# Kernel tuning notes

Hardware: AMD Instinct MI355X
Metric: run time of the kernel (lower is better)

Reference implementation:

```python
import jax, jax.numpy as jnp
import numpy as np

RES = (160, 160, 160)
SCENE_MIN = -1.0
SCENE_SIZE = 2.0
NEAR, FAR = 0.1, 10.0
NUM_SAMPLES = 128


def eval_sh_deg2(dirs):
    # dirs: [N, 3] -> SH basis [N, 9] (degree 2)
    d = dirs / (jnp.linalg.norm(dirs, axis=-1, keepdims=True) + 1e-8)
    x, y, z = d[..., 0], d[..., 1], d[..., 2]
    return jnp.stack([
        0.28209479177387814 * jnp.ones_like(x),
        -0.48860251190291987 * y,
        0.48860251190291987 * z,
        -0.48860251190291987 * x,
        1.0925484305920792 * x * y,
        -1.0925484305920792 * y * z,
        0.31539156525252005 * (2.0 * z * z - x * x - y * y),
        -1.0925484305920792 * x * z,
        0.5462742152960396 * (x * x - y * y),
    ], axis=-1)


def trilinear_interp(coords, density, sh_coeffs):
    # coords: [N, 3] world coords; grids indexed [z, y, x] as in the torch source
    res = jnp.asarray(RES, dtype=coords.dtype)
    vox = (coords - SCENE_MIN) / SCENE_SIZE * res
    vox = jnp.clip(vox, 0.0, res - 1.0)
    fl = jnp.floor(vox)
    frac = vox - fl
    fl = fl.astype(jnp.int32)
    x0, y0, z0 = fl[..., 0], fl[..., 1], fl[..., 2]
    x1 = jnp.minimum(x0 + 1, RES[0] - 1)
    y1 = jnp.minimum(y0 + 1, RES[1] - 1)
    z1 = jnp.minimum(z0 + 1, RES[2] - 1)
    dx, dy, dz = frac[..., 0], frac[..., 1], frac[..., 2]
    corners = [
        ((z0, y0, x0), (1 - dx) * (1 - dy) * (1 - dz)),
        ((z1, y0, x0), (1 - dx) * (1 - dy) * dz),
        ((z0, y1, x0), (1 - dx) * dy * (1 - dz)),
        ((z1, y1, x0), (1 - dx) * dy * dz),
        ((z0, y0, x1), dx * (1 - dy) * (1 - dz)),
        ((z1, y0, x1), dx * (1 - dy) * dz),
        ((z0, y1, x1), dx * dy * (1 - dz)),
        ((z1, y1, x1), dx * dy * dz),
    ]
    dens = 0.0
    sh = 0.0
    for (zi, yi, xi), w in corners:
        dens = dens + w * density[zi, yi, xi]
        sh = sh + w[:, None, None] * sh_coeffs[zi, yi, xi]
    return dens, sh


def plenoxel_forward(ray_origins, ray_directions, density, sh_coeffs):
    R = ray_origins.shape[0]
    t_vals = jnp.linspace(NEAR, FAR, NUM_SAMPLES, dtype=ray_origins.dtype)  # [S]
    # points: [R, S, 3]
    points = ray_origins[:, None, :] + t_vals[None, :, None] * ray_directions[:, None, :]
    pts = points.reshape(-1, 3)
    dens, sh = trilinear_interp(pts, density, sh_coeffs)  # [N], [N,3,9]
    dirs = jnp.broadcast_to(ray_directions[:, None, :], points.shape).reshape(-1, 3)
    basis = eval_sh_deg2(dirs)  # [N, 9]
    colors = jax.nn.sigmoid(jnp.sum(sh * basis[:, None, :], axis=-1))  # [N, 3]
    dens = dens.reshape(R, NUM_SAMPLES)
    colors = colors.reshape(R, NUM_SAMPLES, 3)
    # volume rendering
    dists = t_vals[1:] - t_vals[:-1]
    dists = jnp.concatenate([dists, jnp.full((1,), 1e10, dtype=t_vals.dtype)], axis=0)
    dists = dists[None, :] * jnp.linalg.norm(ray_directions, axis=-1, keepdims=True)  # [R,S]
    alpha = 1.0 - jnp.exp(-jax.nn.relu(dens) * dists)
    trans = jnp.cumprod(1.0 - alpha + 1e-10, axis=-1)
    trans = jnp.concatenate([jnp.ones_like(trans[..., :1]), trans[..., :-1]], axis=-1)
    weights = alpha * trans
    rgb = jnp.sum(weights[..., None] * colors, axis=-2)  # [R,3]
    depth = jnp.sum(weights * t_vals[None, :], axis=-1)  # [R]
    acc = jnp.sum(weights, axis=-1)  # [R]
    return rgb, depth, acc


def setup_inputs() -> dict:
    key = jax.random.key(0)
    k0, k1, k2, k3 = jax.random.split(key, 4)
    R = 4096
    ray_origins = jax.random.uniform(k0, (R, 3), dtype=jnp.float32, minval=-0.5, maxval=0.5)
    ray_directions = jax.random.normal(k1, (R, 3), dtype=jnp.float32)
    ray_directions = ray_directions / jnp.linalg.norm(ray_directions, axis=-1, keepdims=True)
    density = jax.random.uniform(k2, RES, dtype=jnp.float32, minval=-0.1, maxval=0.1)
    sh_coeffs = jax.random.uniform(k3, (*RES, 3, 9), dtype=jnp.float32, minval=-0.1, maxval=0.1)
    sh_coeffs = sh_coeffs.at[..., 0].set(0.5)
    return {"ray_origins": ray_origins, "ray_directions": ray_directions,
            "density": density, "sh_coeffs": sh_coeffs}


def reference(ray_origins, ray_directions, density, sh_coeffs):
    return plenoxel_forward(ray_origins, ray_directions, density, sh_coeffs)
```

## Files before the change

kernel.cpp:

```cpp
#include <hip/hip_runtime.h>
#include <math.h>

#define RES 160
#define NSAMP 128
#define NEAR_T 0.1f
#define FAR_T 10.0f

typedef float float4v __attribute__((ext_vector_type(4)));

__global__ __launch_bounds__(1024) void plenoxel_kernel(
    const float* __restrict__ ray_o,
    const float* __restrict__ ray_d,
    const float* __restrict__ density,
    const float* __restrict__ sh,
    float* __restrict__ out_rgb,
    float* __restrict__ out_depth,
    float* __restrict__ out_acc,
    int R)
{
    const int r   = blockIdx.x;
    const int tid = threadIdx.x;
    const int s   = tid >> 3;
    const int e   = tid & 7;
    if (r >= R) return;

    const float ox = ray_o[r * 3 + 0], oy = ray_o[r * 3 + 1], oz = ray_o[r * 3 + 2];
    const float dx = ray_d[r * 3 + 0], dy = ray_d[r * 3 + 1], dz = ray_d[r * 3 + 2];

    const float dn  = sqrtf(dx * dx + dy * dy + dz * dz);
    const float inv = 1.0f / (dn + 1e-8f);
    const float nx = dx * inv, ny = dy * inv, nz = dz * inv;
    const float b0 = 0.28209479177387814f;
    const float b1 = -0.48860251190291987f * ny;
    const float b2 =  0.48860251190291987f * nz;
    const float b3 = -0.48860251190291987f * nx;
    const float b4 =  1.0925484305920792f * nx * ny;
    const float b5 = -1.0925484305920792f * ny * nz;
    const float b6 =  0.31539156525252005f * (2.0f * nz * nz - nx * nx - ny * ny);
    const float b7 = -1.0925484305920792f * nx * nz;
    const float b8 =  0.5462742152960396f * (nx * nx - ny * ny);

    float4v bLo = {0.f, 0.f, 0.f, 0.f}, bHi = {0.f, 0.f, 0.f, 0.f};
    int chLo = 3, chHi = 3;
    switch (e) {
        case 0: bLo = (float4v){b0, b1, b2, b3}; chLo = 0; break;
        case 1: bLo = (float4v){b4, b5, b6, b7}; chLo = 0; break;
        case 2: bLo = (float4v){b8, 0.f, 0.f, 0.f}; bHi = (float4v){0.f, b0, b1, b2};
                chLo = 0; chHi = 1; break;
        case 3: bLo = (float4v){b3, b4, b5, b6}; chLo = 1; break;
        case 4: bLo = (float4v){b7, b8, 0.f, 0.f}; bHi = (float4v){0.f, 0.f, b0, b1};
                chLo = 1; chHi = 2; break;
        case 5: bLo = (float4v){b2, b3, b4, b5}; chLo = 2; break;
        case 6: bLo = (float4v){0.f, b6, b7, b8}; chLo = 2; break;
        default: break;
    }
    const int offE = (e >= 6) ? 23 : 4 * e;

    const float step = (FAR_T - NEAR_T) / (float)(NSAMP - 1);
    const float t = NEAR_T + step * (float)s;
    const float px = ox + t * dx, py = oy + t * dy, pz = oz + t * dz;
    float vx = (px + 1.0f) * 0.5f * (float)RES;
    float vy = (py + 1.0f) * 0.5f * (float)RES;
    float vz = (pz + 1.0f) * 0.5f * (float)RES;
    vx = fminf(fmaxf(vx, 0.0f), (float)(RES - 1));
    vy = fminf(fmaxf(vy, 0.0f), (float)(RES - 1));
    vz = fminf(fmaxf(vz, 0.0f), (float)(RES - 1));
    const float flx = floorf(vx), fly = floorf(vy), flz = floorf(vz);
    const int x0 = (int)flx, y0 = (int)fly, z0 = (int)flz;
    const int x1 = min(x0 + 1, RES - 1);
    const int y1 = min(y0 + 1, RES - 1);
    const int z1 = min(z0 + 1, RES - 1);
    const float fx = vx - flx, fy = vy - fly, fz = vz - flz;

    const float wx0 = 1.0f - fx, wx1 = fx;
    const float wy0 = 1.0f - fy, wy1 = fy;
    const float wz0 = 1.0f - fz, wz1 = fz;

    const int zy00 = (z0 * RES + y0) * RES;
    const int zy01 = (z0 * RES + y1) * RES;
    const int zy10 = (z1 * RES + y0) * RES;
    const int zy11 = (z1 * RES + y1) * RES;
    int   vidx[8];
    float w8[8];
    vidx[0] = zy00 + x0; w8[0] = wx0 * wy0 * wz0;
    vidx[1] = zy10 + x0; w8[1] = wx0 * wy0 * wz1;
    vidx[2] = zy01 + x0; w8[2] = wx0 * wy1 * wz0;
    vidx[3] = zy11 + x0; w8[3] = wx0 * wy1 * wz1;
    vidx[4] = zy00 + x1; w8[4] = wx1 * wy0 * wz0;
    vidx[5] = zy10 + x1; w8[5] = wx1 * wy0 * wz1;
    vidx[6] = zy01 + x1; w8[6] = wx1 * wy1 * wz0;
    vidx[7] = zy11 + x1; w8[7] = wx1 * wy1 * wz1;

    float vD = w8[e] * density[vidx[e]];

    float accLo = 0.0f, accHi = 0.0f;
    #pragma unroll
    for (int k = 0; k < 8; ++k) {
        const float* p = sh + (size_t)vidx[k] * 27 + offE;
        float4v row = *(const float4v*)p;
        const float tl = row.x * bLo.x + row.y * bLo.y + row.z * bLo.z + row.w * bLo.w;
        const float th = row.x * bHi.x + row.y * bHi.y + row.z * bHi.z + row.w * bHi.w;
        accLo = fmaf(tl, w8[k], accLo);
        accHi = fmaf(th, w8[k], accHi);
    }

    float v0 = ((chLo == 0) ? accLo : 0.0f) + ((chHi == 0) ? accHi : 0.0f);
    float v1 = ((chLo == 1) ? accLo : 0.0f) + ((chHi == 1) ? accHi : 0.0f);
    float v2 = ((chLo == 2) ? accLo : 0.0f) + ((chHi == 2) ? accHi : 0.0f);
    float v3 = vD;
    #pragma unroll
    for (int m = 1; m < 8; m <<= 1) {
        v0 += __shfl_xor(v0, m, 64);
        v1 += __shfl_xor(v1, m, 64);
        v2 += __shfl_xor(v2, m, 64);
        v3 += __shfl_xor(v3, m, 64);
    }

    __shared__ float4v sdata[NSAMP];
    if (e == 0) sdata[s] = (float4v){v0, v1, v2, v3};
    __syncthreads();

    float incl = 1.0f, alpha = 0.0f, col0 = 0.f, col1 = 0.f, col2 = 0.f, ts = 0.f;
    const int lane = tid & 63;
    if (tid < NSAMP) {
        const float4v d = sdata[tid];
        col0 = 1.0f / (1.0f + __expf(-d.x));
        col1 = 1.0f / (1.0f + __expf(-d.y));
        col2 = 1.0f / (1.0f + __expf(-d.z));
        ts = NEAR_T + step * (float)tid;
        float dist = ((tid == NSAMP - 1) ? 1e10f : step) * dn;
        alpha = 1.0f - __expf(-fmaxf(d.w, 0.0f) * dist);
        const float om = 1.0f - alpha + 1e-10f;
        incl = om;
        #pragma unroll
        for (int off = 1; off < 64; off <<= 1) {
            const float u = __shfl_up(incl, off, 64);
            incl *= (lane >= off) ? u : 1.0f;
        }
    }
    __shared__ float w0tot;
    if (tid == 63) w0tot = incl;
    __syncthreads();

    __shared__ float part[2][5];
    if (tid < NSAMP) {
        float excl = __shfl_up(incl, 1, 64);
        if (lane == 0) excl = 1.0f;
        const float trans = (tid < 64) ? excl : excl * w0tot;
        const float wgt = alpha * trans;
        float u0 = wgt * col0, u1 = wgt * col1, u2 = wgt * col2, u3 = wgt * ts, u4 = wgt;
        #pragma unroll
        for (int off = 32; off > 0; off >>= 1) {
            u0 += __shfl_down(u0, off, 64);
            u1 += __shfl_down(u1, off, 64);
            u2 += __shfl_down(u2, off, 64);
            u3 += __shfl_down(u3, off, 64);
            u4 += __shfl_down(u4, off, 64);
        }
        if (lane == 0) {
            const int wv = tid >> 6;
            part[wv][0] = u0; part[wv][1] = u1; part[wv][2] = u2;
            part[wv][3] = u3; part[wv][4] = u4;
        }
    }
    __syncthreads();
    if (tid == 0) {
        out_rgb[r * 3 + 0] = part[0][0] + part[1][0];
        out_rgb[r * 3 + 1] = part[0][1] + part[1][1];
        out_rgb[r * 3 + 2] = part[0][2] + part[1][2];
        out_depth[r]       = part[0][3] + part[1][3];
        out_acc[r]         = part[0][4] + part[1][4];
    }
}

extern "C" void kernel_launch(void* const* d_in, const int* in_sizes, int n_in,
                              void* d_out, int out_size, void* d_ws, size_t ws_size,
                              hipStream_t stream) {
    const float* ray_o   = (const float*)d_in[0];
    const float* ray_d   = (const float*)d_in[1];
    const float* density = (const float*)d_in[2];
    const float* sh      = (const float*)d_in[3];
    const int R = in_sizes[0] / 3;

    float* out_rgb   = (float*)d_out;
    float* out_depth = out_rgb + (size_t)R * 3;
    float* out_acc   = out_depth + R;

    plenoxel_kernel<<<R, 1024, 0, stream>>>(ray_o, ray_d, density, sh,
                                            out_rgb, out_depth, out_acc, R);
}
```

Measured before the change: 524.4 us.

## Split density and SH passes and fetch SH only for nonzero-weight samples

The kernel now runs the density pass first and computes alpha, transmittance and weights. Using a ballot and prefix count, it builds a compacted list of samples whose weight is nonzero, and only those samples gather the 27-float SH coefficients at their 8 corners. Skipping zero-weight samples is meant to cut the dominant SH gather traffic, since negative densities give zero alpha. In exchange the kernel recomputes sample geometry, adds several block barriers and shared-memory staging, and its benefit depends on how sparse the nonzero weights are.

```diff
diff --git a/kernel.cpp b/kernel.cpp
--- a/kernel.cpp
+++ b/kernel.cpp
@@ -5,8 +5,47 @@
 #define NSAMP 128
 #define NEAR_T 0.1f
 #define FAR_T 10.0f
+#define STEP ((FAR_T - NEAR_T) / (float)(NSAMP - 1))
 
 typedef float float4v __attribute__((ext_vector_type(4)));
+
+__device__ __forceinline__ void sample_geom(
+    const float ox, const float oy, const float oz,
+    const float dx, const float dy, const float dz,
+    const int s, int vidx[8], float w8[8])
+{
+    const float t = NEAR_T + STEP * (float)s;
+    const float px = ox + t * dx, py = oy + t * dy, pz = oz + t * dz;
+    float vx = (px + 1.0f) * 0.5f * (float)RES;
+    float vy = (py + 1.0f) * 0.5f * (float)RES;
+    float vz = (pz + 1.0f) * 0.5f * (float)RES;
+    vx = fminf(fmaxf(vx, 0.0f), (float)(RES - 1));
+    vy = fminf(fmaxf(vy, 0.0f), (float)(RES - 1));
+    vz = fminf(fmaxf(vz, 0.0f), (float)(RES - 1));
+    const float flx = floorf(vx), fly = floorf(vy), flz = floorf(vz);
+    const int x0 = (int)flx, y0 = (int)fly, z0 = (int)flz;
+    const int x1 = min(x0 + 1, RES - 1);
+    const int y1 = min(y0 + 1, RES - 1);
+    const int z1 = min(z0 + 1, RES - 1);
+    const float fx = vx - flx, fy = vy - fly, fz = vz - flz;
+
+    const float wx0 = 1.0f - fx, wx1 = fx;
+    const float wy0 = 1.0f - fy, wy1 = fy;
+    const float wz0 = 1.0f - fz, wz1 = fz;
+
+    const int zy00 = (z0 * RES + y0) * RES;
+    const int zy01 = (z0 * RES + y1) * RES;
+    const int zy10 = (z1 * RES + y0) * RES;
+    const int zy11 = (z1 * RES + y1) * RES;
+    vidx[0] = zy00 + x0; w8[0] = wx0 * wy0 * wz0;
+    vidx[1] = zy10 + x0; w8[1] = wx0 * wy0 * wz1;
+    vidx[2] = zy01 + x0; w8[2] = wx0 * wy1 * wz0;
+    vidx[3] = zy11 + x0; w8[3] = wx0 * wy1 * wz1;
+    vidx[4] = zy00 + x1; w8[4] = wx1 * wy0 * wz0;
+    vidx[5] = zy10 + x1; w8[5] = wx1 * wy0 * wz1;
+    vidx[6] = zy01 + x1; w8[6] = wx1 * wy1 * wz0;
+    vidx[7] = zy11 + x1; w8[7] = wx1 * wy1 * wz1;
+}
 
 __global__ __launch_bounds__(1024) void plenoxel_kernel(
     const float* __restrict__ ray_o,
@@ -22,7 +61,17 @@
     const int tid = threadIdx.x;
     const int s   = tid >> 3;
     const int e   = tid & 7;
+    const int lane = tid & 63;
     if (r >= R) return;
+
+    __shared__ float  sdens[NSAMP];
+    __shared__ float  swgt[NSAMP];
+    __shared__ int    slist[NSAMP];
+    __shared__ int    scnt[2];
+    __shared__ float  w0tot;
+    __shared__ float  partDA[2][2];
+    __shared__ float  partRGB[2][3];
+    __shared__ float4v srgb[NSAMP];
 
     const float ox = ray_o[r * 3 + 0], oy = ray_o[r * 3 + 1], oz = ray_o[r * 3 + 2];
     const float dx = ray_d[r * 3 + 0], dy = ray_d[r * 3 + 1], dz = ray_d[r * 3 + 2];
@@ -56,81 +105,24 @@
     }
     const int offE = (e >= 6) ? 23 : 4 * e;
 
-    const float step = (FAR_T - NEAR_T) / (float)(NSAMP - 1);
-    const float t = NEAR_T + step * (float)s;
-    const float px = ox + t * dx, py = oy + t * dy, pz = oz + t * dz;
-    float vx = (px + 1.0f) * 0.5f * (float)RES;
-    float vy = (py + 1.0f) * 0.5f * (float)RES;
-    float vz = (pz + 1.0f) * 0.5f * (float)RES;
-    vx = fminf(fmaxf(vx, 0.0f), (float)(RES - 1));
-    vy = fminf(fmaxf(vy, 0.0f), (float)(RES - 1));
-    vz = fminf(fmaxf(vz, 0.0f), (float)(RES - 1));
-    const float flx = floorf(vx), fly = floorf(vy), flz = floorf(vz);
-    const int x0 = (int)flx, y0 = (int)fly, z0 = (int)flz;
-    const int x1 = min(x0 + 1, RES - 1);
-    const int y1 = min(y0 + 1, RES - 1);
-    const int z1 = min(z0 + 1, RES - 1);
-    const float fx = vx - flx, fy = vy - fly, fz = vz - flz;
-
-    const float wx0 = 1.0f - fx, wx1 = fx;
-    const float wy0 = 1.0f - fy, wy1 = fy;
-    const float wz0 = 1.0f - fz, wz1 = fz;
-
-    const int zy00 = (z0 * RES + y0) * RES;
-    const int zy01 = (z0 * RES + y1) * RES;
-    const int zy10 = (z1 * RES + y0) * RES;
-    const int zy11 = (z1 * RES + y1) * RES;
-    int   vidx[8];
-    float w8[8];
-    vidx[0] = zy00 + x0; w8[0] = wx0 * wy0 * wz0;
-    vidx[1] = zy10 + x0; w8[1] = wx0 * wy0 * wz1;
-    vidx[2] = zy01 + x0; w8[2] = wx0 * wy1 * wz0;
-    vidx[3] = zy11 + x0; w8[3] = wx0 * wy1 * wz1;
-    vidx[4] = zy00 + x1; w8[4] = wx1 * wy0 * wz0;
-    vidx[5] = zy10 + x1; w8[5] = wx1 * wy0 * wz1;
-    vidx[6] = zy01 + x1; w8[6] = wx1 * wy1 * wz0;
-    vidx[7] = zy11 + x1; w8[7] = wx1 * wy1 * wz1;
-
-    float vD = w8[e] * density[vidx[e]];
-
-    float accLo = 0.0f, accHi = 0.0f;
-    #pragma unroll
-    for (int k = 0; k < 8; ++k) {
-        const float* p = sh + (size_t)vidx[k] * 27 + offE;
-        float4v row = *(const float4v*)p;
-        const float tl = row.x * bLo.x + row.y * bLo.y + row.z * bLo.z + row.w * bLo.w;
-        const float th = row.x * bHi.x + row.y * bHi.y + row.z * bHi.z + row.w * bHi.w;
-        accLo = fmaf(tl, w8[k], accLo);
-        accHi = fmaf(th, w8[k], accHi);
-    }
-
-    float v0 = ((chLo == 0) ? accLo : 0.0f) + ((chHi == 0) ? accHi : 0.0f);
-    float v1 = ((chLo == 1) ? accLo : 0.0f) + ((chHi == 1) ? accHi : 0.0f);
-    float v2 = ((chLo == 2) ? accLo : 0.0f) + ((chHi == 2) ? accHi : 0.0f);
-    float v3 = vD;
-    #pragma unroll
-    for (int m = 1; m < 8; m <<= 1) {
-        v0 += __shfl_xor(v0, m, 64);
-        v1 += __shfl_xor(v1, m, 64);
-        v2 += __shfl_xor(v2, m, 64);
-        v3 += __shfl_xor(v3, m, 64);
-    }
-
-    __shared__ float4v sdata[NSAMP];
-    if (e == 0) sdata[s] = (float4v){v0, v1, v2, v3};
-    __syncthreads();
-
-    float incl = 1.0f, alpha = 0.0f, col0 = 0.f, col1 = 0.f, col2 = 0.f, ts = 0.f;
-    const int lane = tid & 63;
+    {
+        int vidx[8]; float w8[8];
+        sample_geom(ox, oy, oz, dx, dy, dz, s, vidx, w8);
+        float vD = w8[e] * density[vidx[e]];
+        #pragma unroll
+        for (int m = 1; m < 8; m <<= 1) vD += __shfl_xor(vD, m, 64);
+        if (e == 0) sdens[s] = vD;
+    }
+    __syncthreads();
+
+    float incl = 1.0f, alphaV = 0.0f, tsV = 0.0f, wgt = 0.0f;
+    bool flag = false; int rank = 0;
     if (tid < NSAMP) {
-        const float4v d = sdata[tid];
-        col0 = 1.0f / (1.0f + __expf(-d.x));
-        col1 = 1.0f / (1.0f + __expf(-d.y));
-        col2 = 1.0f / (1.0f + __expf(-d.z));
-        ts = NEAR_T + step * (float)tid;
-        float dist = ((tid == NSAMP - 1) ? 1e10f : step) * dn;
-        alpha = 1.0f - __expf(-fmaxf(d.w, 0.0f) * dist);
-        const float om = 1.0f - alpha + 1e-10f;
+        const float d = sdens[tid];
+        tsV = NEAR_T + STEP * (float)tid;
+        const float dist = ((tid == NSAMP - 1) ? 1e10f : STEP) * dn;
+        alphaV = 1.0f - __expf(-fmaxf(d, 0.0f) * dist);
+        const float om = 1.0f - alphaV + 1e-10f;
         incl = om;
         #pragma unroll
         for (int off = 1; off < 64; off <<= 1) {
@@ -138,38 +130,95 @@
             incl *= (lane >= off) ? u : 1.0f;
         }
     }
-    __shared__ float w0tot;
     if (tid == 63) w0tot = incl;
     __syncthreads();
 
-    __shared__ float part[2][5];
     if (tid < NSAMP) {
         float excl = __shfl_up(incl, 1, 64);
         if (lane == 0) excl = 1.0f;
         const float trans = (tid < 64) ? excl : excl * w0tot;
-        const float wgt = alpha * trans;
-        float u0 = wgt * col0, u1 = wgt * col1, u2 = wgt * col2, u3 = wgt * ts, u4 = wgt;
+        wgt = alphaV * trans;
+        swgt[tid] = wgt;
+        flag = (wgt != 0.0f);
+        const unsigned long long mask = __ballot(flag);
+        rank = __popcll(mask & ((1ull << lane) - 1ull));
+        if (lane == 0) scnt[tid >> 6] = __popcll(mask);
+        float u3 = wgt * tsV, u4 = wgt;
+        #pragma unroll
+        for (int off = 32; off > 0; off >>= 1) {
+            u3 += __shfl_down(u3, off, 64);
+            u4 += __shfl_down(u4, off, 64);
+        }
+        if (lane == 0) { partDA[tid >> 6][0] = u3; partDA[tid >> 6][1] = u4; }
+    }
+    __syncthreads();
+
+    if (tid < NSAMP && flag) {
+        const int base = (tid >= 64) ? scnt[0] : 0;
+        slist[base + rank] = tid;
+    }
+    __syncthreads();
+    const int S = scnt[0] + scnt[1];
+
+    const int g = tid >> 3;
+    float rgb0 = 0.f, rgb1 = 0.f, rgb2 = 0.f;
+    if (g < S) {
+        const int s2 = slist[g];
+        int vidx[8]; float w8[8];
+        sample_geom(ox, oy, oz, dx, dy, dz, s2, vidx, w8);
+
+        float accLo = 0.0f, accHi = 0.0f;
+        if (e < 7) {
+            #pragma unroll
+            for (int k = 0; k < 8; ++k) {
+                const float* p = sh + (size_t)vidx[k] * 27 + offE;
+                float4v row = *(const float4v*)p;
+                const float tl = row.x * bLo.x + row.y * bLo.y + row.z * bLo.z + row.w * bLo.w;
+                const float th = row.x * bHi.x + row.y * bHi.y + row.z * bHi.z + row.w * bHi.w;
+                accLo = fmaf(tl, w8[k], accLo);
+                accHi = fmaf(th, w8[k], accHi);
+            }
+        }
+        float v0 = ((chLo == 0) ? accLo : 0.0f) + ((chHi == 0) ? accHi : 0.0f);
+        float v1 = ((chLo == 1) ? accLo : 0.0f) + ((chHi == 1) ? accHi : 0.0f);
+        float v2 = ((chLo == 2) ? accLo : 0.0f) + ((chHi == 2) ? accHi : 0.0f);
+        #pragma unroll
+        for (int m = 1; m < 8; m <<= 1) {
+            v0 += __shfl_xor(v0, m, 64);
+            v1 += __shfl_xor(v1, m, 64);
+            v2 += __shfl_xor(v2, m, 64);
+        }
+        if (e == 0) {
+            const float wg = swgt[s2];
+            rgb0 = wg * (1.0f / (1.0f + __expf(-v0)));
+            rgb1 = wg * (1.0f / (1.0f + __expf(-v1)));
+            rgb2 = wg * (1.0f / (1.0f + __expf(-v2)));
+        }
+    }
+    if (e == 0) srgb[g] = (float4v){rgb0, rgb1, rgb2, 0.f};
+    __syncthreads();
+
+    if (tid < NSAMP) {
+        const float4v dd = srgb[tid];
+        float u0 = dd.x, u1 = dd.y, u2 = dd.z;
         #pragma unroll
         for (int off = 32; off > 0; off >>= 1) {
             u0 += __shfl_down(u0, off, 64);
             u1 += __shfl_down(u1, off, 64);
             u2 += __shfl_down(u2, off, 64);
-            u3 += __shfl_down(u3, off, 64);
-            u4 += __shfl_down(u4, off, 64);
         }
         if (lane == 0) {
             const int wv = tid >> 6;
-            part[wv][0] = u0; part[wv][1] = u1; part[wv][2] = u2;
-            part[wv][3] = u3; part[wv][4] = u4;
+            partRGB[wv][0] = u0; partRGB[wv][1] = u1; partRGB[wv][2] = u2;
         }
     }
     __syncthreads();
     if (tid == 0) {
-        out_rgb[r * 3 + 0] = part[0][0] + part[1][0];
-        out_rgb[r * 3 + 1] = part[0][1] + part[1][1];
-        out_rgb[r * 3 + 2] = part[0][2] + part[1][2];
-        out_depth[r]       = part[0][3] + part[1][3];
-        out_acc[r]         = part[0][4] + part[1][4];
+        out_rgb[r * 3 + 0] = partRGB[0][0] + partRGB[1][0];
+        out_rgb[r * 3 + 1] = partRGB[0][1] + partRGB[1][1];
+        out_rgb[r * 3 + 2] = partRGB[0][2] + partRGB[1][2];
+        out_depth[r]       = partDA[0][0] + partDA[1][0];
+        out_acc[r]         = partDA[0][1] + partDA[1][1];
     }
 }
 
```

After: 556.6 us. 6.2% more time.

## Compute density first, then gather SH only for samples with nonzero weight

Applied to the files above, without the earlier changes.

The kernel is restructured so one 64-thread wave handles a ray. Each lane first computes density and alpha for two samples and runs the transmittance scan. Samples whose weight is nonzero are then compacted with ballot/popcount into a shared list, and the 8-lane groups loop over that list to do the 27-float SH gathers and sigmoid. The aim is to skip the expensive SH corner loads for samples that contribute exactly zero (negative density or zero transmittance). The cost is less parallelism per ray: sample processing becomes a serial loop, and density corner loads are duplicated in the geometry recompute.

```diff
diff --git a/kernel.cpp b/kernel.cpp
--- a/kernel.cpp
+++ b/kernel.cpp
@@ -5,10 +5,49 @@
 #define NSAMP 128
 #define NEAR_T 0.1f
 #define FAR_T 10.0f
+#define STEP ((FAR_T - NEAR_T) / (float)(NSAMP - 1))
 
 typedef float float4v __attribute__((ext_vector_type(4)));
 
-__global__ __launch_bounds__(1024) void plenoxel_kernel(
+__device__ __forceinline__ void sample_geom8(
+    const float ox, const float oy, const float oz,
+    const float dx, const float dy, const float dz,
+    const int s, int vidx[8], float w8[8])
+{
+    const float t = NEAR_T + STEP * (float)s;
+    const float px = ox + t * dx, py = oy + t * dy, pz = oz + t * dz;
+    float vx = (px + 1.0f) * 0.5f * (float)RES;
+    float vy = (py + 1.0f) * 0.5f * (float)RES;
+    float vz = (pz + 1.0f) * 0.5f * (float)RES;
+    vx = fminf(fmaxf(vx, 0.0f), (float)(RES - 1));
+    vy = fminf(fmaxf(vy, 0.0f), (float)(RES - 1));
+    vz = fminf(fmaxf(vz, 0.0f), (float)(RES - 1));
+    const float flx = floorf(vx), fly = floorf(vy), flz = floorf(vz);
+    const int x0 = (int)flx, y0 = (int)fly, z0 = (int)flz;
+    const int x1 = min(x0 + 1, RES - 1);
+    const int y1 = min(y0 + 1, RES - 1);
+    const int z1 = min(z0 + 1, RES - 1);
+    const float fx = vx - flx, fy = vy - fly, fz = vz - flz;
+
+    const float wx0 = 1.0f - fx, wx1 = fx;
+    const float wy0 = 1.0f - fy, wy1 = fy;
+    const float wz0 = 1.0f - fz, wz1 = fz;
+
+    const int zy00 = (z0 * RES + y0) * RES;
+    const int zy01 = (z0 * RES + y1) * RES;
+    const int zy10 = (z1 * RES + y0) * RES;
+    const int zy11 = (z1 * RES + y1) * RES;
+    vidx[0] = zy00 + x0; w8[0] = wx0 * wy0 * wz0;
+    vidx[1] = zy10 + x0; w8[1] = wx0 * wy0 * wz1;
+    vidx[2] = zy01 + x0; w8[2] = wx0 * wy1 * wz0;
+    vidx[3] = zy11 + x0; w8[3] = wx0 * wy1 * wz1;
+    vidx[4] = zy00 + x1; w8[4] = wx1 * wy0 * wz0;
+    vidx[5] = zy10 + x1; w8[5] = wx1 * wy0 * wz1;
+    vidx[6] = zy01 + x1; w8[6] = wx1 * wy1 * wz0;
+    vidx[7] = zy11 + x1; w8[7] = wx1 * wy1 * wz1;
+}
+
+__global__ __launch_bounds__(64) void plenoxel_kernel(
     const float* __restrict__ ray_o,
     const float* __restrict__ ray_d,
     const float* __restrict__ density,
@@ -18,11 +57,14 @@
     float* __restrict__ out_acc,
     int R)
 {
-    const int r   = blockIdx.x;
-    const int tid = threadIdx.x;
-    const int s   = tid >> 3;
-    const int e   = tid & 7;
+    const int r    = blockIdx.x;
+    const int lane = threadIdx.x;
+    const int g    = lane >> 3;
+    const int e    = lane & 7;
     if (r >= R) return;
+
+    __shared__ float swgt[NSAMP];
+    __shared__ int   slist[NSAMP];
 
     const float ox = ray_o[r * 3 + 0], oy = ray_o[r * 3 + 1], oz = ray_o[r * 3 + 2];
     const float dx = ray_d[r * 3 + 0], dy = ray_d[r * 3 + 1], dz = ray_d[r * 3 + 2];
@@ -56,120 +98,104 @@
     }
     const int offE = (e >= 6) ? 23 : 4 * e;
 
-    const float step = (FAR_T - NEAR_T) / (float)(NSAMP - 1);
-    const float t = NEAR_T + step * (float)s;
-    const float px = ox + t * dx, py = oy + t * dy, pz = oz + t * dz;
-    float vx = (px + 1.0f) * 0.5f * (float)RES;
-    float vy = (py + 1.0f) * 0.5f * (float)RES;
-    float vz = (pz + 1.0f) * 0.5f * (float)RES;
-    vx = fminf(fmaxf(vx, 0.0f), (float)(RES - 1));
-    vy = fminf(fmaxf(vy, 0.0f), (float)(RES - 1));
-    vz = fminf(fmaxf(vz, 0.0f), (float)(RES - 1));
-    const float flx = floorf(vx), fly = floorf(vy), flz = floorf(vz);
-    const int x0 = (int)flx, y0 = (int)fly, z0 = (int)flz;
-    const int x1 = min(x0 + 1, RES - 1);
-    const int y1 = min(y0 + 1, RES - 1);
-    const int z1 = min(z0 + 1, RES - 1);
-    const float fx = vx - flx, fy = vy - fly, fz = vz - flz;
-
-    const float wx0 = 1.0f - fx, wx1 = fx;
-    const float wy0 = 1.0f - fy, wy1 = fy;
-    const float wz0 = 1.0f - fz, wz1 = fz;
-
-    const int zy00 = (z0 * RES + y0) * RES;
-    const int zy01 = (z0 * RES + y1) * RES;
-    const int zy10 = (z1 * RES + y0) * RES;
-    const int zy11 = (z1 * RES + y1) * RES;
-    int   vidx[8];
-    float w8[8];
-    vidx[0] = zy00 + x0; w8[0] = wx0 * wy0 * wz0;
-    vidx[1] = zy10 + x0; w8[1] = wx0 * wy0 * wz1;
-    vidx[2] = zy01 + x0; w8[2] = wx0 * wy1 * wz0;
-    vidx[3] = zy11 + x0; w8[3] = wx0 * wy1 * wz1;
-    vidx[4] = zy00 + x1; w8[4] = wx1 * wy0 * wz0;
-    vidx[5] = zy10 + x1; w8[5] = wx1 * wy0 * wz1;
-    vidx[6] = zy01 + x1; w8[6] = wx1 * wy1 * wz0;
-    vidx[7] = zy11 + x1; w8[7] = wx1 * wy1 * wz1;
-
-    float vD = w8[e] * density[vidx[e]];
-
-    float accLo = 0.0f, accHi = 0.0f;
+    float d0 = 0.0f, d1 = 0.0f;
+    {
+        int vA[8], vB[8]; float wA[8], wB[8];
+        sample_geom8(ox, oy, oz, dx, dy, dz, 2 * lane,     vA, wA);
+        sample_geom8(ox, oy, oz, dx, dy, dz, 2 * lane + 1, vB, wB);
+        #pragma unroll
+        for (int k = 0; k < 8; ++k) d0 = fmaf(wA[k], density[vA[k]], d0);
+        #pragma unroll
+        for (int k = 0; k < 8; ++k) d1 = fmaf(wB[k], density[vB[k]], d1);
+    }
+
+    const float t0 = NEAR_T + STEP * (float)(2 * lane);
+    const float t1 = t0 + STEP;
+    const float dist0 = STEP * dn;
+    const float dist1 = ((lane == 63) ? 1e10f : STEP) * dn;
+    const float a0 = 1.0f - __expf(-fmaxf(d0, 0.0f) * dist0);
+    const float a1 = 1.0f - __expf(-fmaxf(d1, 0.0f) * dist1);
+    const float om0 = 1.0f - a0 + 1e-10f;
+    const float om1 = 1.0f - a1 + 1e-10f;
+
+    float incl = om0 * om1;
     #pragma unroll
-    for (int k = 0; k < 8; ++k) {
-        const float* p = sh + (size_t)vidx[k] * 27 + offE;
-        float4v row = *(const float4v*)p;
-        const float tl = row.x * bLo.x + row.y * bLo.y + row.z * bLo.z + row.w * bLo.w;
-        const float th = row.x * bHi.x + row.y * bHi.y + row.z * bHi.z + row.w * bHi.w;
-        accLo = fmaf(tl, w8[k], accLo);
-        accHi = fmaf(th, w8[k], accHi);
-    }
-
-    float v0 = ((chLo == 0) ? accLo : 0.0f) + ((chHi == 0) ? accHi : 0.0f);
-    float v1 = ((chLo == 1) ? accLo : 0.0f) + ((chHi == 1) ? accHi : 0.0f);
-    float v2 = ((chLo == 2) ? accLo : 0.0f) + ((chHi == 2) ? accHi : 0.0f);
-    float v3 = vD;
+    for (int off = 1; off < 64; off <<= 1) {
+        const float u = __shfl_up(incl, off, 64);
+        incl *= (lane >= off) ? u : 1.0f;
+    }
+    float excl = __shfl_up(incl, 1, 64);
+    if (lane == 0) excl = 1.0f;
+    const float w0 = a0 * excl;
+    const float w1 = a1 * excl * om0;
+
+    float accD = w0 * t0 + w1 * t1;
+    float accA = w0 + w1;
+
+    const bool f0 = (w0 != 0.0f), f1 = (w1 != 0.0f);
+    const unsigned long long m0 = __ballot(f0);
+    const unsigned long long m1 = __ballot(f1);
+    const unsigned long long below = (1ull << lane) - 1ull;
+    const int nb = __popcll(m0 & below) + __popcll(m1 & below);
+    const int S  = __popcll(m0) + __popcll(m1);
+    if (f0) slist[nb] = 2 * lane;
+    if (f1) slist[nb + (f0 ? 1 : 0)] = 2 * lane + 1;
+    swgt[2 * lane]     = w0;
+    swgt[2 * lane + 1] = w1;
+    __syncthreads();
+
+    float rgb0 = 0.f, rgb1 = 0.f, rgb2 = 0.f;
+    const int nIter = (S + 7) >> 3;
+    for (int i = 0; i < nIter; ++i) {
+        const int gi = i * 8 + g;
+        const int s2 = (gi < S) ? slist[gi] : slist[0];
+        int vidx[8]; float w8[8];
+        sample_geom8(ox, oy, oz, dx, dy, dz, s2, vidx, w8);
+
+        float accLo = 0.0f, accHi = 0.0f;
+        if (e < 7 && gi < S) {
+            #pragma unroll
+            for (int k = 0; k < 8; ++k) {
+                const float* p = sh + (size_t)vidx[k] * 27 + offE;
+                float4v row = *(const float4v*)p;
+                const float tl = row.x * bLo.x + row.y * bLo.y + row.z * bLo.z + row.w * bLo.w;
+                const float th = row.x * bHi.x + row.y * bHi.y + row.z * bHi.z + row.w * bHi.w;
+                accLo = fmaf(tl, w8[k], accLo);
+                accHi = fmaf(th, w8[k], accHi);
+            }
+        }
+        float v0 = ((chLo == 0) ? accLo : 0.0f) + ((chHi == 0) ? accHi : 0.0f);
+        float v1 = ((chLo == 1) ? accLo : 0.0f) + ((chHi == 1) ? accHi : 0.0f);
+        float v2 = ((chLo == 2) ? accLo : 0.0f) + ((chHi == 2) ? accHi : 0.0f);
+        #pragma unroll
+        for (int m = 1; m < 8; m <<= 1) {
+            v0 += __shfl_xor(v0, m, 64);
+            v1 += __shfl_xor(v1, m, 64);
+            v2 += __shfl_xor(v2, m, 64);
+        }
+        if (e == 0 && gi < S) {
+            const float wg = swgt[s2];
+            rgb0 = fmaf(wg, 1.0f / (1.0f + __expf(-v0)), rgb0);
+            rgb1 = fmaf(wg, 1.0f / (1.0f + __expf(-v1)), rgb1);
+            rgb2 = fmaf(wg, 1.0f / (1.0f + __expf(-v2)), rgb2);
+        }
+    }
+
+    float u0 = rgb0, u1 = rgb1, u2 = rgb2, u3 = accD, u4 = accA;
     #pragma unroll
-    for (int m = 1; m < 8; m <<= 1) {
-        v0 += __shfl_xor(v0, m, 64);
-        v1 += __shfl_xor(v1, m, 64);
-        v2 += __shfl_xor(v2, m, 64);
-        v3 += __shfl_xor(v3, m, 64);
-    }
-
-    __shared__ float4v sdata[NSAMP];
-    if (e == 0) sdata[s] = (float4v){v0, v1, v2, v3};
-    __syncthreads();
-
-    float incl = 1.0f, alpha = 0.0f, col0 = 0.f, col1 = 0.f, col2 = 0.f, ts = 0.f;
-    const int lane = tid & 63;
-    if (tid < NSAMP) {
-        const float4v d = sdata[tid];
-        col0 = 1.0f / (1.0f + __expf(-d.x));
-        col1 = 1.0f / (1.0f + __expf(-d.y));
-        col2 = 1.0f / (1.0f + __expf(-d.z));
-        ts = NEAR_T + step * (float)tid;
-        float dist = ((tid == NSAMP - 1) ? 1e10f : step) * dn;
-        alpha = 1.0f - __expf(-fmaxf(d.w, 0.0f) * dist);
-        const float om = 1.0f - alpha + 1e-10f;
-        incl = om;
-        #pragma unroll
-        for (int off = 1; off < 64; off <<= 1) {
-            const float u = __shfl_up(incl, off, 64);
-            incl *= (lane >= off) ? u : 1.0f;
-        }
-    }
-    __shared__ float w0tot;
-    if (tid == 63) w0tot = incl;
-    __syncthreads();
-
-    __shared__ float part[2][5];
-    if (tid < NSAMP) {
-        float excl = __shfl_up(incl, 1, 64);
-        if (lane == 0) excl = 1.0f;
-        const float trans = (tid < 64) ? excl : excl * w0tot;
-        const float wgt = alpha * trans;
-        float u0 = wgt * col0, u1 = wgt * col1, u2 = wgt * col2, u3 = wgt * ts, u4 = wgt;
-        #pragma unroll
-        for (int off = 32; off > 0; off >>= 1) {
-            u0 += __shfl_down(u0, off, 64);
-            u1 += __shfl_down(u1, off, 64);
-            u2 += __shfl_down(u2, off, 64);
-            u3 += __shfl_down(u3, off, 64);
-            u4 += __shfl_down(u4, off, 64);
-        }
-        if (lane == 0) {
-            const int wv = tid >> 6;
-            part[wv][0] = u0; part[wv][1] = u1; part[wv][2] = u2;
-            part[wv][3] = u3; part[wv][4] = u4;
-        }
-    }
-    __syncthreads();
-    if (tid == 0) {
-        out_rgb[r * 3 + 0] = part[0][0] + part[1][0];
-        out_rgb[r * 3 + 1] = part[0][1] + part[1][1];
-        out_rgb[r * 3 + 2] = part[0][2] + part[1][2];
-        out_depth[r]       = part[0][3] + part[1][3];
-        out_acc[r]         = part[0][4] + part[1][4];
+    for (int off = 32; off > 0; off >>= 1) {
+        u0 += __shfl_down(u0, off, 64);
+        u1 += __shfl_down(u1, off, 64);
+        u2 += __shfl_down(u2, off, 64);
+        u3 += __shfl_down(u3, off, 64);
+        u4 += __shfl_down(u4, off, 64);
+    }
+    if (lane == 0) {
+        out_rgb[r * 3 + 0] = u0;
+        out_rgb[r * 3 + 1] = u1;
+        out_rgb[r * 3 + 2] = u2;
+        out_depth[r]       = u3;
+        out_acc[r]         = u4;
     }
 }
 
@@ -186,6 +212,6 @@
     float* out_depth = out_rgb + (size_t)R * 3;
     float* out_acc   = out_depth + R;
 
-    plenoxel_kernel<<<R, 1024, 0, stream>>>(ray_o, ray_d, density, sh,
-                                            out_rgb, out_depth, out_acc, R);
+    plenoxel_kernel<<<R, 64, 0, stream>>>(ray_o, ray_d, density, sh,
+                                          out_rgb, out_depth, out_acc, R);
 }
```

Result: no change. 517.0 us (-1.4%).

## Compact nonzero-weight samples and gather SH only for them with double buffering

Applied to the files above, without the earlier changes.

Restructures the kernel into two phases. First, 128 threads compute density and compositing weights per sample. Then ballot-based compaction builds a list of samples with nonzero weight, and only those samples gather and evaluate SH coefficients in a software-pipelined double-buffered loop. This avoids SH gathers for samples whose density clamps to zero, at the cost of extra synchronisation, recomputation of sample geometry and higher register pressure.

```diff
diff --git a/kernel.cpp b/kernel.cpp
--- a/kernel.cpp
+++ b/kernel.cpp
@@ -5,10 +5,49 @@
 #define NSAMP 128
 #define NEAR_T 0.1f
 #define FAR_T 10.0f
+#define STEP ((FAR_T - NEAR_T) / (float)(NSAMP - 1))
 
 typedef float float4v __attribute__((ext_vector_type(4)));
 
-__global__ __launch_bounds__(1024) void plenoxel_kernel(
+__device__ __forceinline__ void sample_geom8(
+    const float ox, const float oy, const float oz,
+    const float dx, const float dy, const float dz,
+    const int s, int vidx[8], float w8[8])
+{
+    const float t = NEAR_T + STEP * (float)s;
+    const float px = ox + t * dx, py = oy + t * dy, pz = oz + t * dz;
+    float vx = (px + 1.0f) * 0.5f * (float)RES;
+    float vy = (py + 1.0f) * 0.5f * (float)RES;
+    float vz = (pz + 1.0f) * 0.5f * (float)RES;
+    vx = fminf(fmaxf(vx, 0.0f), (float)(RES - 1));
+    vy = fminf(fmaxf(vy, 0.0f), (float)(RES - 1));
+    vz = fminf(fmaxf(vz, 0.0f), (float)(RES - 1));
+    const float flx = floorf(vx), fly = floorf(vy), flz = floorf(vz);
+    const int x0 = (int)flx, y0 = (int)fly, z0 = (int)flz;
+    const int x1 = min(x0 + 1, RES - 1);
+    const int y1 = min(y0 + 1, RES - 1);
+    const int z1 = min(z0 + 1, RES - 1);
+    const float fx = vx - flx, fy = vy - fly, fz = vz - flz;
+
+    const float wx0 = 1.0f - fx, wx1 = fx;
+    const float wy0 = 1.0f - fy, wy1 = fy;
+    const float wz0 = 1.0f - fz, wz1 = fz;
+
+    const int zy00 = (z0 * RES + y0) * RES;
+    const int zy01 = (z0 * RES + y1) * RES;
+    const int zy10 = (z1 * RES + y0) * RES;
+    const int zy11 = (z1 * RES + y1) * RES;
+    vidx[0] = zy00 + x0; w8[0] = wx0 * wy0 * wz0;
+    vidx[1] = zy10 + x0; w8[1] = wx0 * wy0 * wz1;
+    vidx[2] = zy01 + x0; w8[2] = wx0 * wy1 * wz0;
+    vidx[3] = zy11 + x0; w8[3] = wx0 * wy1 * wz1;
+    vidx[4] = zy00 + x1; w8[4] = wx1 * wy0 * wz0;
+    vidx[5] = zy10 + x1; w8[5] = wx1 * wy0 * wz1;
+    vidx[6] = zy01 + x1; w8[6] = wx1 * wy1 * wz0;
+    vidx[7] = zy11 + x1; w8[7] = wx1 * wy1 * wz1;
+}
+
+__global__ __launch_bounds__(128, 4) void plenoxel_kernel(
     const float* __restrict__ ray_o,
     const float* __restrict__ ray_d,
     const float* __restrict__ density,
@@ -18,11 +57,20 @@
     float* __restrict__ out_acc,
     int R)
 {
-    const int r   = blockIdx.x;
-    const int tid = threadIdx.x;
-    const int s   = tid >> 3;
-    const int e   = tid & 7;
+    const int r    = blockIdx.x;
+    const int tid  = threadIdx.x;
+    const int wv   = tid >> 6;
+    const int lane = tid & 63;
+    const int g2   = tid >> 3;
+    const int e    = tid & 7;
     if (r >= R) return;
+
+    __shared__ float swgt[NSAMP];
+    __shared__ int   slist[NSAMP];
+    __shared__ int   scnt[2];
+    __shared__ float w0tot;
+    __shared__ float partDA[2][2];
+    __shared__ float partRGB[2][3];
 
     const float ox = ray_o[r * 3 + 0], oy = ray_o[r * 3 + 1], oz = ray_o[r * 3 + 2];
     const float dx = ray_d[r * 3 + 0], dy = ray_d[r * 3 + 1], dz = ray_d[r * 3 + 2];
@@ -56,120 +104,134 @@
     }
     const int offE = (e >= 6) ? 23 : 4 * e;
 
-    const float step = (FAR_T - NEAR_T) / (float)(NSAMP - 1);
-    const float t = NEAR_T + step * (float)s;
-    const float px = ox + t * dx, py = oy + t * dy, pz = oz + t * dz;
-    float vx = (px + 1.0f) * 0.5f * (float)RES;
-    float vy = (py + 1.0f) * 0.5f * (float)RES;
-    float vz = (pz + 1.0f) * 0.5f * (float)RES;
-    vx = fminf(fmaxf(vx, 0.0f), (float)(RES - 1));
-    vy = fminf(fmaxf(vy, 0.0f), (float)(RES - 1));
-    vz = fminf(fmaxf(vz, 0.0f), (float)(RES - 1));
-    const float flx = floorf(vx), fly = floorf(vy), flz = floorf(vz);
-    const int x0 = (int)flx, y0 = (int)fly, z0 = (int)flz;
-    const int x1 = min(x0 + 1, RES - 1);
-    const int y1 = min(y0 + 1, RES - 1);
-    const int z1 = min(z0 + 1, RES - 1);
-    const float fx = vx - flx, fy = vy - fly, fz = vz - flz;
-
-    const float wx0 = 1.0f - fx, wx1 = fx;
-    const float wy0 = 1.0f - fy, wy1 = fy;
-    const float wz0 = 1.0f - fz, wz1 = fz;
-
-    const int zy00 = (z0 * RES + y0) * RES;
-    const int zy01 = (z0 * RES + y1) * RES;
-    const int zy10 = (z1 * RES + y0) * RES;
-    const int zy11 = (z1 * RES + y1) * RES;
-    int   vidx[8];
-    float w8[8];
-    vidx[0] = zy00 + x0; w8[0] = wx0 * wy0 * wz0;
-    vidx[1] = zy10 + x0; w8[1] = wx0 * wy0 * wz1;
-    vidx[2] = zy01 + x0; w8[2] = wx0 * wy1 * wz0;
-    vidx[3] = zy11 + x0; w8[3] = wx0 * wy1 * wz1;
-    vidx[4] = zy00 + x1; w8[4] = wx1 * wy0 * wz0;
-    vidx[5] = zy10 + x1; w8[5] = wx1 * wy0 * wz1;
-    vidx[6] = zy01 + x1; w8[6] = wx1 * wy1 * wz0;
-    vidx[7] = zy11 + x1; w8[7] = wx1 * wy1 * wz1;
-
-    float vD = w8[e] * density[vidx[e]];
-
-    float accLo = 0.0f, accHi = 0.0f;
+    float dsum = 0.0f;
+    {
+        int vidx[8]; float w8[8];
+        sample_geom8(ox, oy, oz, dx, dy, dz, tid, vidx, w8);
+        #pragma unroll
+        for (int k = 0; k < 8; ++k) dsum = fmaf(w8[k], density[vidx[k]], dsum);
+    }
+
+    const float ts   = NEAR_T + STEP * (float)tid;
+    const float dist = ((tid == NSAMP - 1) ? 1e10f : STEP) * dn;
+    const float alpha = 1.0f - __expf(-fmaxf(dsum, 0.0f) * dist);
+    const float om = 1.0f - alpha + 1e-10f;
+
+    float incl = om;
     #pragma unroll
-    for (int k = 0; k < 8; ++k) {
-        const float* p = sh + (size_t)vidx[k] * 27 + offE;
-        float4v row = *(const float4v*)p;
-        const float tl = row.x * bLo.x + row.y * bLo.y + row.z * bLo.z + row.w * bLo.w;
-        const float th = row.x * bHi.x + row.y * bHi.y + row.z * bHi.z + row.w * bHi.w;
-        accLo = fmaf(tl, w8[k], accLo);
-        accHi = fmaf(th, w8[k], accHi);
-    }
-
-    float v0 = ((chLo == 0) ? accLo : 0.0f) + ((chHi == 0) ? accHi : 0.0f);
-    float v1 = ((chLo == 1) ? accLo : 0.0f) + ((chHi == 1) ? accHi : 0.0f);
-    float v2 = ((chLo == 2) ? accLo : 0.0f) + ((chHi == 2) ? accHi : 0.0f);
-    float v3 = vD;
-    #pragma unroll
-    for (int m = 1; m < 8; m <<= 1) {
-        v0 += __shfl_xor(v0, m, 64);
-        v1 += __shfl_xor(v1, m, 64);
-        v2 += __shfl_xor(v2, m, 64);
-        v3 += __shfl_xor(v3, m, 64);
-    }
-
-    __shared__ float4v sdata[NSAMP];
-    if (e == 0) sdata[s] = (float4v){v0, v1, v2, v3};
-    __syncthreads();
-
-    float incl = 1.0f, alpha = 0.0f, col0 = 0.f, col1 = 0.f, col2 = 0.f, ts = 0.f;
-    const int lane = tid & 63;
-    if (tid < NSAMP) {
-        const float4v d = sdata[tid];
-        col0 = 1.0f / (1.0f + __expf(-d.x));
-        col1 = 1.0f / (1.0f + __expf(-d.y));
-        col2 = 1.0f / (1.0f + __expf(-d.z));
-        ts = NEAR_T + step * (float)tid;
-        float dist = ((tid == NSAMP - 1) ? 1e10f : step) * dn;
-        alpha = 1.0f - __expf(-fmaxf(d.w, 0.0f) * dist);
-        const float om = 1.0f - alpha + 1e-10f;
-        incl = om;
+    for (int off = 1; off < 64; off <<= 1) {
+        const float u = __shfl_up(incl, off, 64);
+        incl *= (lane >= off) ? u : 1.0f;
+    }
+    if (tid == 63) w0tot = incl;
+    __syncthreads();
+
+    float excl = __shfl_up(incl, 1, 64);
+    if (lane == 0) excl = 1.0f;
+    const float scale = wv ? w0tot : 1.0f;
+    const float wgt = alpha * excl * scale;
+    swgt[tid] = wgt;
+
+    {
+        float u3 = wgt * ts, u4 = wgt;
         #pragma unroll
-        for (int off = 1; off < 64; off <<= 1) {
-            const float u = __shfl_up(incl, off, 64);
-            incl *= (lane >= off) ? u : 1.0f;
-        }
-    }
-    __shared__ float w0tot;
-    if (tid == 63) w0tot = incl;
-    __syncthreads();
-
-    __shared__ float part[2][5];
-    if (tid < NSAMP) {
-        float excl = __shfl_up(incl, 1, 64);
-        if (lane == 0) excl = 1.0f;
-        const float trans = (tid < 64) ? excl : excl * w0tot;
-        const float wgt = alpha * trans;
-        float u0 = wgt * col0, u1 = wgt * col1, u2 = wgt * col2, u3 = wgt * ts, u4 = wgt;
+        for (int off = 32; off > 0; off >>= 1) {
+            u3 += __shfl_down(u3, off, 64);
+            u4 += __shfl_down(u4, off, 64);
+        }
+        if (lane == 0) { partDA[wv][0] = u3; partDA[wv][1] = u4; }
+    }
+
+    const bool flag = (wgt != 0.0f);
+    const unsigned long long mask = __ballot(flag);
+    const int rank = __popcll(mask & ((1ull << lane) - 1ull));
+    if (lane == 0) scnt[wv] = __popcll(mask);
+    __syncthreads();
+    const int base = wv ? scnt[0] : 0;
+    if (flag) slist[base + rank] = tid;
+    __syncthreads();
+    const int S = scnt[0] + scnt[1];
+
+    float rgb0 = 0.f, rgb1 = 0.f, rgb2 = 0.f;
+    const int nIter = (S + 15) >> 4;
+
+    float4v rA[8] = {}; float wA[8]; int s2A = 0; bool vA_ = false;
+    float4v rB[8] = {}; float wB[8]; int s2B = 0; bool vB_ = false;
+
+#define SH_LOAD(J, S2, WW, RR, VV) do {                                        \
+        const int gi_ = (J) * 16 + g2;                                         \
+        VV = (gi_ < S);                                                        \
+        S2 = VV ? slist[gi_] : 0;                                              \
+        int vidx_[8];                                                          \
+        sample_geom8(ox, oy, oz, dx, dy, dz, S2, vidx_, WW);                   \
+        if (VV && e < 7) {                                                     \
+            _Pragma("unroll")                                                  \
+            for (int k_ = 0; k_ < 8; ++k_)                                     \
+                RR[k_] = *(const float4v*)(sh + (size_t)vidx_[k_] * 27 + offE);\
+        }                                                                      \
+    } while (0)
+
+#define SH_COMPUTE(S2, WW, RR, VV) do {                                        \
+        float accLo_ = 0.f, accHi_ = 0.f;                                      \
+        _Pragma("unroll")                                                      \
+        for (int k_ = 0; k_ < 8; ++k_) {                                       \
+            const float tl_ = RR[k_].x * bLo.x + RR[k_].y * bLo.y +            \
+                              RR[k_].z * bLo.z + RR[k_].w * bLo.w;             \
+            const float th_ = RR[k_].x * bHi.x + RR[k_].y * bHi.y +            \
+                              RR[k_].z * bHi.z + RR[k_].w * bHi.w;             \
+            accLo_ = fmaf(tl_, WW[k_], accLo_);                                \
+            accHi_ = fmaf(th_, WW[k_], accHi_);                                \
+        }                                                                      \
+        float v0_ = ((chLo == 0) ? accLo_ : 0.f) + ((chHi == 0) ? accHi_ : 0.f);\
+        float v1_ = ((chLo == 1) ? accLo_ : 0.f) + ((chHi == 1) ? accHi_ : 0.f);\
+        float v2_ = ((chLo == 2) ? accLo_ : 0.f) + ((chHi == 2) ? accHi_ : 0.f);\
+        _Pragma("unroll")                                                      \
+        for (int m_ = 1; m_ < 8; m_ <<= 1) {                                   \
+            v0_ += __shfl_xor(v0_, m_, 64);                                    \
+            v1_ += __shfl_xor(v1_, m_, 64);                                    \
+            v2_ += __shfl_xor(v2_, m_, 64);                                    \
+        }                                                                      \
+        if (e == 0 && VV) {                                                    \
+            const float wg_ = swgt[S2];                                        \
+            rgb0 = fmaf(wg_, 1.0f / (1.0f + __expf(-v0_)), rgb0);              \
+            rgb1 = fmaf(wg_, 1.0f / (1.0f + __expf(-v1_)), rgb1);              \
+            rgb2 = fmaf(wg_, 1.0f / (1.0f + __expf(-v2_)), rgb2);              \
+        }                                                                      \
+    } while (0)
+
+    if (nIter > 0) {
+        SH_LOAD(0, s2A, wA, rA, vA_);
+        for (int i = 0; i < nIter; i += 2) {
+            if (i + 1 < nIter) SH_LOAD(i + 1, s2B, wB, rB, vB_);
+            SH_COMPUTE(s2A, wA, rA, vA_);
+            if (i + 1 < nIter) {
+                if (i + 2 < nIter) SH_LOAD(i + 2, s2A, wA, rA, vA_);
+                SH_COMPUTE(s2B, wB, rB, vB_);
+            }
+        }
+    }
+#undef SH_LOAD
+#undef SH_COMPUTE
+
+    {
+        float u0 = rgb0, u1 = rgb1, u2 = rgb2;
         #pragma unroll
         for (int off = 32; off > 0; off >>= 1) {
             u0 += __shfl_down(u0, off, 64);
             u1 += __shfl_down(u1, off, 64);
             u2 += __shfl_down(u2, off, 64);
-            u3 += __shfl_down(u3, off, 64);
-            u4 += __shfl_down(u4, off, 64);
         }
         if (lane == 0) {
-            const int wv = tid >> 6;
-            part[wv][0] = u0; part[wv][1] = u1; part[wv][2] = u2;
-            part[wv][3] = u3; part[wv][4] = u4;
+            partRGB[wv][0] = u0; partRGB[wv][1] = u1; partRGB[wv][2] = u2;
         }
     }
     __syncthreads();
     if (tid == 0) {
-        out_rgb[r * 3 + 0] = part[0][0] + part[1][0];
-        out_rgb[r * 3 + 1] = part[0][1] + part[1][1];
-        out_rgb[r * 3 + 2] = part[0][2] + part[1][2];
-        out_depth[r]       = part[0][3] + part[1][3];
-        out_acc[r]         = part[0][4] + part[1][4];
+        out_rgb[r * 3 + 0] = partRGB[0][0] + partRGB[1][0];
+        out_rgb[r * 3 + 1] = partRGB[0][1] + partRGB[1][1];
+        out_rgb[r * 3 + 2] = partRGB[0][2] + partRGB[1][2];
+        out_depth[r]       = partDA[0][0] + partDA[1][0];
+        out_acc[r]         = partDA[0][1] + partDA[1][1];
     }
 }
 
@@ -186,6 +248,6 @@
     float* out_depth = out_rgb + (size_t)R * 3;
     float* out_acc   = out_depth + R;
 
-    plenoxel_kernel<<<R, 1024, 0, stream>>>(ray_o, ray_d, density, sh,
-                                            out_rgb, out_depth, out_acc, R);
+    plenoxel_kernel<<<R, 128, 0, stream>>>(ray_o, ray_d, density, sh,
+                                           out_rgb, out_depth, out_acc, R);
 }
```

New measurement: 509.4 us. 2.9% less time.
